# Optimization experiments

Hardware: AMD Instinct MI355X
Metric: run time of the kernel (lower is better)

## Reference

```python
import jax, jax.numpy as jnp
import numpy as np

N, M, F = 2048, 512, 256

def setup_inputs() -> dict:
    key = jax.random.key(0)
    k1, k2, k3, k4 = jax.random.split(key, 4)
    noteFea = jax.random.normal(k1, (N, F), dtype=jnp.float32)
    labFea = jax.random.normal(k2, (M, F), dtype=jnp.float32)
    # nn.Linear(featureSize, 1): weight [1, F] -> store as [F]; bias [1]
    bound = 1.0 / np.sqrt(F)
    W = jax.random.uniform(k3, (F,), dtype=jnp.float32, minval=-bound, maxval=bound)
    b = jax.random.uniform(k4, (1,), dtype=jnp.float32, minval=-bound, maxval=bound)
    return {"noteFea": noteFea, "labFea": labFea, "W": W, "b": b}

def reference(noteFea, labFea, W, b):
    # dis = noteFea[:,None,:] - labFea[None,:,:]  -> [N, M, F]
    # out = Linear(dis).squeeze(-1)               -> [N, M]
    dis = noteFea[:, None, :] - labFea[None, :, :]
    return jnp.einsum('nmf,f->nm', dis, W) + b[0]
```

## Files before the change

kernel.cpp:

```cpp
#include <hip/hip_runtime.h>


#define N_ROWS 2048
#define M_ROWS 512
#define FDIM   256

__global__ void siamese_dots(const float* __restrict__ note,
                             const float* __restrict__ lab,
                             const float* __restrict__ W,
                             float* __restrict__ ws) {
    int gid  = blockIdx.x * blockDim.x + threadIdx.x;
    int wave = gid >> 6;
    int lane = threadIdx.x & 63;
    const int total = N_ROWS + M_ROWS;
    if (wave >= total) return;

    const float* row = (wave < N_ROWS)
        ? note + (size_t)wave * FDIM
        : lab  + (size_t)(wave - N_ROWS) * FDIM;

    float4 v = reinterpret_cast<const float4*>(row)[lane];
    float4 w = reinterpret_cast<const float4*>(W)[lane];
    float s = v.x * w.x + v.y * w.y + v.z * w.z + v.w * w.w;

    #pragma unroll
    for (int off = 32; off > 0; off >>= 1)
        s += __shfl_down(s, off, 64);

    if (lane == 0) ws[wave] = s;
}

__global__ void siamese_fill(const float* __restrict__ ws,
                             const float* __restrict__ bptr,
                             float* __restrict__ out) {
    int idx = blockIdx.x * blockDim.x + threadIdx.x;
    int mq  = idx & (M_ROWS / 4 - 1);
    int n   = idx >> 7;

    float a  = ws[n];
    float4 c = reinterpret_cast<const float4*>(ws + N_ROWS)[mq];
    float bb = bptr[0];

    float4 o;
    o.x = a - c.x + bb;
    o.y = a - c.y + bb;
    o.z = a - c.z + bb;
    o.w = a - c.w + bb;
    reinterpret_cast<float4*>(out)[idx] = o;
}

extern "C" void kernel_launch(void* const* d_in, const int* in_sizes, int n_in,
                              void* d_out, int out_size, void* d_ws, size_t ws_size,
                              hipStream_t stream) {
    const float* note = (const float*)d_in[0];
    const float* lab  = (const float*)d_in[1];
    const float* W    = (const float*)d_in[2];
    const float* b    = (const float*)d_in[3];
    float* out        = (float*)d_out;
    float* ws         = (float*)d_ws;

    {
        const int total_waves = N_ROWS + M_ROWS;
        const int block = 256;
        const int waves_per_block = block / 64;
        const int grid = (total_waves + waves_per_block - 1) / waves_per_block;
        siamese_dots<<<grid, block, 0, stream>>>(note, lab, W, ws);
    }

    {
        const int total = N_ROWS * (M_ROWS / 4);
        const int block = 256;
        const int grid = total / block;
        siamese_fill<<<grid, block, 0, stream>>>(ws, b, out);
    }
}
```

Measured before the change: 11.61 us.

## Fuse dot-product and broadcast-fill kernels into one with redundant lab dots per block

Merges the two launches into a single kernel. Each block computes the W-dots for its 8 note rows, recomputes all 512 lab-row dots itself, and then writes its 8x512 output tile from shared memory. This removes the second launch and the workspace round trip. The cost is that all 256 blocks each read the full 512 KB lab matrix, with every thread walking one row serially and uncoalesced, which adds a lot of redundant L2 traffic and compute.

```diff
diff --git a/kernel.cpp b/kernel.cpp
--- a/kernel.cpp
+++ b/kernel.cpp
@@ -4,49 +4,73 @@
 #define N_ROWS 2048
 #define M_ROWS 512
 #define FDIM   256
+#define RPB    8
+#define NBLK   (N_ROWS / RPB)
 
-__global__ void siamese_dots(const float* __restrict__ note,
-                             const float* __restrict__ lab,
-                             const float* __restrict__ W,
-                             float* __restrict__ ws) {
-    int gid  = blockIdx.x * blockDim.x + threadIdx.x;
-    int wave = gid >> 6;
-    int lane = threadIdx.x & 63;
-    const int total = N_ROWS + M_ROWS;
-    if (wave >= total) return;
+__global__ __launch_bounds__(256)
+void siamese_fused(const float* __restrict__ note,
+                   const float* __restrict__ lab,
+                   const float* __restrict__ W,
+                   const float* __restrict__ bptr,
+                   float* __restrict__ out) {
+    __shared__ float s_w[FDIM];
+    __shared__ float s_c[M_ROWS];
+    __shared__ float s_a[RPB];
 
-    const float* row = (wave < N_ROWS)
-        ? note + (size_t)wave * FDIM
-        : lab  + (size_t)(wave - N_ROWS) * FDIM;
+    const int t    = threadIdx.x;
+    const int blk  = blockIdx.x;
+    const int wave = t >> 6;
+    const int lane = t & 63;
 
-    float4 v = reinterpret_cast<const float4*>(row)[lane];
-    float4 w = reinterpret_cast<const float4*>(W)[lane];
-    float s = v.x * w.x + v.y * w.y + v.z * w.z + v.w * w.w;
+    if (t < 64) {
+        reinterpret_cast<float4*>(s_w)[t] = reinterpret_cast<const float4*>(W)[t];
+    }
+    __syncthreads();
 
     #pragma unroll
-    for (int off = 32; off > 0; off >>= 1)
-        s += __shfl_down(s, off, 64);
+    for (int rr = wave; rr < RPB; rr += 4) {
+        const int n = blk * RPB + rr;
+        float4 v = reinterpret_cast<const float4*>(note + (size_t)n * FDIM)[lane];
+        float4 w = reinterpret_cast<const float4*>(s_w)[lane];
+        float s = v.x * w.x + v.y * w.y + v.z * w.z + v.w * w.w;
+        #pragma unroll
+        for (int off = 32; off > 0; off >>= 1)
+            s += __shfl_down(s, off, 64);
+        if (lane == 0) s_a[rr] = s;
+    }
 
-    if (lane == 0) ws[wave] = s;
-}
+    #pragma unroll
+    for (int mm = 0; mm < 2; ++mm) {
+        const int m = t + mm * 256;
+        const float4* row = reinterpret_cast<const float4*>(lab + (size_t)m * FDIM);
+        float acc = 0.0f;
+        #pragma unroll 8
+        for (int j = 0; j < FDIM / 4; ++j) {
+            float4 v = row[j];
+            float4 w = reinterpret_cast<const float4*>(s_w)[j];
+            acc += v.x * w.x + v.y * w.y + v.z * w.z + v.w * w.w;
+        }
+        s_c[m] = acc;
+    }
 
-__global__ void siamese_fill(const float* __restrict__ ws,
-                             const float* __restrict__ bptr,
-                             float* __restrict__ out) {
-    int idx = blockIdx.x * blockDim.x + threadIdx.x;
-    int mq  = idx & (M_ROWS / 4 - 1);
-    int n   = idx >> 7;
+    __syncthreads();
 
-    float a  = ws[n];
-    float4 c = reinterpret_cast<const float4*>(ws + N_ROWS)[mq];
-    float bb = bptr[0];
-
-    float4 o;
-    o.x = a - c.x + bb;
-    o.y = a - c.y + bb;
-    o.z = a - c.z + bb;
-    o.w = a - c.w + bb;
-    reinterpret_cast<float4*>(out)[idx] = o;
+    const float bb = bptr[0];
+    float4* out4 = reinterpret_cast<float4*>(out + (size_t)blk * RPB * M_ROWS);
+    #pragma unroll
+    for (int k = 0; k < 4; ++k) {
+        const int idx = k * 256 + t;
+        const int r   = idx >> 7;
+        const int mq  = idx & 127;
+        const float  a = s_a[r];
+        const float4 c = reinterpret_cast<const float4*>(s_c)[mq];
+        float4 o;
+        o.x = a - c.x + bb;
+        o.y = a - c.y + bb;
+        o.z = a - c.z + bb;
+        o.w = a - c.w + bb;
+        out4[idx] = o;
+    }
 }
 
 extern "C" void kernel_launch(void* const* d_in, const int* in_sizes, int n_in,
@@ -57,20 +81,6 @@
     const float* W    = (const float*)d_in[2];
     const float* b    = (const float*)d_in[3];
     float* out        = (float*)d_out;
-    float* ws         = (float*)d_ws;
 
-    {
-        const int total_waves = N_ROWS + M_ROWS;
-        const int block = 256;
-        const int waves_per_block = block / 64;
-        const int grid = (total_waves + waves_per_block - 1) / waves_per_block;
-        siamese_dots<<<grid, block, 0, stream>>>(note, lab, W, ws);
-    }
-
-    {
-        const int total = N_ROWS * (M_ROWS / 4);
-        const int block = 256;
-        const int grid = total / block;
-        siamese_fill<<<grid, block, 0, stream>>>(ws, b, out);
-    }
+    siamese_fused<<<NBLK, 256, 0, stream>>>(note, lab, W, b, out);
 }
```

Result: slower. 22.06 us (+90.0%).
